# Kernel tuning notes

Hardware: AMD Instinct MI355X
Metric: run time of the kernel (lower is better)

The kernel has to match this reference:

```python
import jax, jax.numpy as jnp
import numpy as np

B, T, C = 2, 2048, 2048
N_HEADS = 16
D_HEAD = C // N_HEADS


def setup_inputs() -> dict:
    key = jax.random.key(0)
    k1, k2, k3 = jax.random.split(key, 3)
    x = jax.random.normal(k1, (B, T, C), dtype=jnp.float32)
    # torch Linear weights stored as [out,in]; we store transposed [in,out] for x @ W
    Wqkv = jax.random.normal(k2, (C, 3 * C), dtype=jnp.float32) * (C ** -0.5)
    Wout = jax.random.normal(k3, (C, C), dtype=jnp.float32) * (C ** -0.5)
    # causal mask: scores where mask==0 are set to -inf
    mask = jnp.tril(jnp.ones((T, T), dtype=bool))[None, None]  # [1,1,T,T]
    return {"x": x, "mask": mask, "Wqkv": Wqkv, "Wout": Wout}


def reference(x, mask, Wqkv, Wout):
    Bx, Tx, Cx = x.shape
    qkv = x @ Wqkv                                   # [B,T,3C]
    q, k, v = jnp.split(qkv, 3, axis=-1)

    def split_heads(t):
        return t.reshape(Bx, Tx, N_HEADS, D_HEAD).transpose(0, 2, 1, 3)  # [B,H,T,Dh]

    q, k, v = split_heads(q), split_heads(k), split_heads(v)
    scale = D_HEAD ** -0.5
    scores = jnp.einsum('bhqd,bhkd->bhqk', q, k) * scale   # [B,H,T,T]
    scores = jnp.where(mask, scores, -jnp.inf)
    attn = jax.nn.softmax(scores, axis=-1)
    # dropout p=0.0 -> identity
    out = jnp.einsum('bhqk,bhkd->bhqd', attn, v)           # [B,H,T,Dh]
    out = out.transpose(0, 2, 1, 3).reshape(Bx, Tx, Cx)
    return out @ Wout
```

## Files before the change

kernel.cpp:

```cpp
#include <hip/hip_runtime.h>
#include <stdint.h>

typedef __bf16 bf16x8 __attribute__((ext_vector_type(8)));
typedef float f32x4 __attribute__((ext_vector_type(4)));
typedef unsigned short u16x8 __attribute__((ext_vector_type(8)));
typedef unsigned int u32x4 __attribute__((ext_vector_type(4)));

__device__ __forceinline__ unsigned short f2bf(float f) {
    unsigned int u = __builtin_bit_cast(unsigned int, f);
    unsigned int r = u + 0x7fffu + ((u >> 16) & 1u);
    return (unsigned short)(r >> 16);
}

__device__ __forceinline__ unsigned int cvt_pk_bf16(float a, float b) {
    unsigned int r;
    asm("v_cvt_pk_bf16_f32 %0, %1, %2" : "=v"(r) : "v"(a), "v"(b));
    return r;
}

__device__ __forceinline__ void async16(const void* g, void* l) {
    __builtin_amdgcn_global_load_lds(
        (const __attribute__((address_space(1))) void*)g,
        (__attribute__((address_space(3))) void*)l, 16, 0, 0);
}


__device__ __forceinline__ void cast_body(
    const float* __restrict__ src, unsigned short* __restrict__ dst, int i)
{
    const float* f = src + (size_t)i * 8;
    f32x4 a = *reinterpret_cast<const f32x4*>(f);
    f32x4 b = *reinterpret_cast<const f32x4*>(f + 4);
    u16x8 r;
    r[0]=f2bf(a[0]); r[1]=f2bf(a[1]); r[2]=f2bf(a[2]); r[3]=f2bf(a[3]);
    r[4]=f2bf(b[0]); r[5]=f2bf(b[1]); r[6]=f2bf(b[2]); r[7]=f2bf(b[3]);
    *reinterpret_cast<u16x8*>(dst + (size_t)i * 8) = r;
}

__device__ __forceinline__ void tcast_body(
    const float* __restrict__ src, unsigned short* __restrict__ dst,
    int R, int Cc, int bx, int by, int tid, unsigned short* St)
{
    const int r0 = by * 64, c0 = bx * 64;
    const int lr  = tid >> 2;
    const int lcb = (tid & 3) * 16;
    const float* sp = src + (size_t)(r0 + lr) * Cc + c0 + lcb;
    #pragma unroll
    for (int u = 0; u < 4; u++) {
        f32x4 v = *reinterpret_cast<const f32x4*>(sp + 4 * u);
        #pragma unroll
        for (int e = 0; e < 4; e++) {
            int c = lcb + 4 * u + e;
            St[c * 64 + (((lr >> 3) ^ ((c >> 4) & 3)) << 3) + (lr & 7)] = f2bf(v[e]);
        }
    }
    __syncthreads();
    #pragma unroll
    for (int i = 0; i < 2; i++) {
        int ck = tid + 256 * i;
        int c = ck >> 3, ch = ck & 7;
        u16x8 val = *reinterpret_cast<const u16x8*>(&St[c * 64 + ((ch ^ ((c >> 4) & 3)) << 3)]);
        *reinterpret_cast<u16x8*>(dst + (size_t)(c0 + c) * R + r0 + ch * 8) = val;
    }
}

__device__ __forceinline__ void vtrans_body(
    const unsigned short* __restrict__ qkv, unsigned short* __restrict__ VT,
    int tx, int dy, int bh, int tid, unsigned short* St)
{
    const int T = 2048, CH = 6144;
    const int b = bh >> 4, h = bh & 15;
    const int t0 = tx * 64, d0 = dy * 64;
    const int lr  = tid >> 2;
    const int lcb = (tid & 3) * 16;
    const unsigned short* sp = qkv + (size_t)(b * T + t0 + lr) * CH + 4096 + h * 128 + d0 + lcb;
    u16x8 v0 = *reinterpret_cast<const u16x8*>(sp);
    u16x8 v1 = *reinterpret_cast<const u16x8*>(sp + 8);
    #pragma unroll
    for (int e = 0; e < 8; e++) {
        int c = lcb + e;
        St[c * 64 + (((lr >> 3) ^ ((c >> 4) & 3)) << 3) + (lr & 7)] = v0[e];
        c = lcb + 8 + e;
        St[c * 64 + (((lr >> 3) ^ ((c >> 4) & 3)) << 3) + (lr & 7)] = v1[e];
    }
    __syncthreads();
    #pragma unroll
    for (int i = 0; i < 2; i++) {
        int ck = tid + 256 * i;
        int d = ck >> 3, ch = ck & 7;
        const int Q = ch & 3, B32 = ch >> 2;
        u16x8 val;
        #pragma unroll
        for (int e = 0; e < 4; e++) {
            int ta = 32 * B32 + 4 * Q + e;
            int tb = ta + 16;
            val[e]     = St[d * 64 + (((ta >> 3) ^ ((d >> 4) & 3)) << 3) + (ta & 7)];
            val[4 + e] = St[d * 64 + (((tb >> 3) ^ ((d >> 4) & 3)) << 3) + (tb & 7)];
        }
        *reinterpret_cast<u16x8*>(VT + (size_t)(bh * 128 + d0 + d) * T + t0 + ch * 8) = val;
    }
}

__global__ __launch_bounds__(256) void prep1(
    const float* __restrict__ x, unsigned short* __restrict__ xb,
    const float* __restrict__ Wqkv, unsigned short* __restrict__ WqkvT)
{
    __shared__ unsigned short St[64 * 64];
    const int bid = blockIdx.x, tid = threadIdx.x;
    if (bid < 4096) {
        cast_body(x, xb, bid * 256 + tid);
    } else {
        const int b2 = bid - 4096;
        tcast_body(Wqkv, WqkvT, 2048, 6144, b2 % 96, b2 / 96, tid, St);
    }
}

__global__ __launch_bounds__(256) void prep2(
    const unsigned short* __restrict__ qkv, unsigned short* __restrict__ VT,
    const float* __restrict__ Wout, unsigned short* __restrict__ WoutT)
{
    __shared__ unsigned short St[64 * 64];
    const int bid = blockIdx.x, tid = threadIdx.x;
    if (bid < 2048) {
        vtrans_body(qkv, VT, bid % 32, (bid >> 5) & 1, bid >> 6, tid, St);
    } else {
        const int b2 = bid - 2048;
        tcast_body(Wout, WoutT, 2048, 2048, b2 % 32, b2 / 32, tid, St);
    }
}

__global__ __launch_bounds__(256) void gemm_bt(
    const unsigned short* __restrict__ A,
    const unsigned short* __restrict__ BT,
    void* __restrict__ C, int M, int N, int K, int cF32)
{
    __shared__ unsigned short As[2][128 * 32];
    __shared__ unsigned short Bs[2][128 * 32];
    const int tid = threadIdx.x;
    const int w = tid >> 6, lane = tid & 63;
    const int quad = lane >> 4, l16 = lane & 15;
    const int wm = (w >> 1) * 64, wn = (w & 1) * 64;
    const int m0 = blockIdx.y * 128, n0 = blockIdx.x * 128;

    const int srow = w * 16 + (lane >> 2);
    const int scol = ((lane & 3) ^ ((lane >> 3) & 3)) * 8;
    const unsigned short* aG = A  + (size_t)(m0 + srow) * K + scol;
    const unsigned short* bG = BT + (size_t)(n0 + srow) * K + scol;
    const int ldsO = (w * 16) * 32;

    const int kch = (quad ^ ((l16 >> 1) & 3)) * 8;

    f32x4 acc[4][4] = {};
    const int nkt = K >> 5;

    async16(aG, &As[0][ldsO]);
    async16(aG + (size_t)64 * K, &As[0][ldsO + 64 * 32]);
    async16(bG, &Bs[0][ldsO]);
    async16(bG + (size_t)64 * K, &Bs[0][ldsO + 64 * 32]);
    asm volatile("s_waitcnt vmcnt(0)\n\ts_barrier" ::: "memory");

    int ct = 0;
    for (int t = 0; t < nkt; ++t) {
        if (t + 1 < nkt) {
            const int k1 = (t + 1) * 32;
            async16(aG + k1, &As[ct ^ 1][ldsO]);
            async16(aG + (size_t)64 * K + k1, &As[ct ^ 1][ldsO + 64 * 32]);
            async16(bG + k1, &Bs[ct ^ 1][ldsO]);
            async16(bG + (size_t)64 * K + k1, &Bs[ct ^ 1][ldsO + 64 * 32]);
        }

        bf16x8 af[4], bf[4];
        #pragma unroll
        for (int i = 0; i < 4; i++)
            af[i] = *reinterpret_cast<const bf16x8*>(&As[ct][(wm + i * 16 + l16) * 32 + kch]);
        #pragma unroll
        for (int c = 0; c < 4; c++)
            bf[c] = *reinterpret_cast<const bf16x8*>(&Bs[ct][(wn + c * 16 + l16) * 32 + kch]);

        __builtin_amdgcn_s_setprio(1);
        #pragma unroll
        for (int i = 0; i < 4; i++)
            #pragma unroll
            for (int c = 0; c < 4; c++)
                acc[i][c] = __builtin_amdgcn_mfma_f32_16x16x32_bf16(af[i], bf[c], acc[i][c], 0, 0, 0);
        __builtin_amdgcn_s_setprio(0);

        asm volatile("s_waitcnt vmcnt(0) lgkmcnt(0)\n\ts_barrier" ::: "memory");
        ct ^= 1;
    }

    #pragma unroll
    for (int i = 0; i < 4; i++)
        #pragma unroll
        for (int c = 0; c < 4; c++)
            #pragma unroll
            for (int r = 0; r < 4; r++) {
                const int row = m0 + wm + i * 16 + quad * 4 + r;
                const int col = n0 + wn + c * 16 + l16;
                const size_t off = (size_t)row * N + col;
                if (cF32) ((float*)C)[off] = acc[i][c][r];
                else ((unsigned short*)C)[off] = f2bf(acc[i][c][r]);
            }
}

__global__ __launch_bounds__(256, 2) void flash_attn(
    const unsigned short* __restrict__ qkv,
    const unsigned short* __restrict__ VT,
    unsigned short* __restrict__ Out)
{
    const int T = 2048, CH = 6144;
    __shared__ unsigned short KsBuf[2][64 * 128];
    __shared__ unsigned short VtBuf[2][128 * 64];

    const int tid = threadIdx.x;
    const int w = tid >> 6, lane = tid & 63;
    const int quad = lane >> 4, l16 = lane & 15;
    const int bh = blockIdx.y, b = bh >> 4, h = bh & 15;
    const int q0 = (gridDim.x - 1 - blockIdx.x) * 128;

    const float sc = 0.08838834764831845f * 1.4426950408889634f;
    const float NINF = -__builtin_inff();

    bf16x8 qf[2][4];
    #pragma unroll
    for (int st = 0; st < 2; st++) {
        const unsigned short* qrow = qkv + (size_t)(b * T + q0 + w * 32 + st * 16 + l16) * CH + h * 128;
        #pragma unroll
        for (int dc = 0; dc < 4; dc++) {
            u16x8 raw = *reinterpret_cast<const u16x8*>(qrow + dc * 32 + quad * 8);
            u16x8 scl;
            #pragma unroll
            for (int e = 0; e < 8; e++) {
                float f = __builtin_bit_cast(float, (unsigned int)raw[e] << 16);
                scl[e] = f2bf(f * sc);
            }
            qf[st][dc] = __builtin_bit_cast(bf16x8, scl);
        }
    }

    f32x4 o[2][8] = {};
    float m_i[2] = {NINF, NINF};
    float l_i[2] = {0.f, 0.f};
    const int xsw = l16 & 7;

    const int kRow = (lane >> 4);
    const int kCh  = lane & 15;
    const int vRow = (lane >> 3);
    const int vCh  = lane & 7;

    auto stageKV = [&](int kv0, unsigned short* kp, unsigned short* vp) {
        #pragma unroll
        for (int i = 0; i < 4; i++) {
            const int r0 = i * 16 + w * 4;
            const int kv = r0 + kRow;
            const int ch = kCh ^ (kv & 7);
            async16(qkv + (size_t)(b * T + kv0 + kv) * CH + 2048 + h * 128 + ch * 8,
                    kp + r0 * 128);
        }
        #pragma unroll
        for (int i = 0; i < 4; i++) {
            const int r0 = i * 32 + w * 8;
            const int d = r0 + vRow;
            const int ch = vCh ^ (d & 7);
            async16(VT + ((size_t)bh * 128 + d) * T + kv0 + ch * 8,
                    vp + r0 * 64);
        }
    };

    unsigned short* kc = KsBuf[0];
    unsigned short* vc = VtBuf[0];
    unsigned short* kn = KsBuf[1];
    unsigned short* vn = VtBuf[1];

    const int nt = (q0 + 128) / 64;

    stageKV(0, kc, vc);
    asm volatile("s_waitcnt vmcnt(0)\n\ts_barrier" ::: "memory");

    for (int t = 0; t < nt; ++t) {
        const int kv0 = t * 64;
        if (t + 1 < nt) stageKV((t + 1) * 64, kn, vn);

        f32x4 s[2][4] = {};
        __builtin_amdgcn_s_setprio(1);
        #pragma unroll
        for (int dc = 0; dc < 4; dc++)
            #pragma unroll
            for (int ntt = 0; ntt < 4; ntt++) {
                bf16x8 kf = *reinterpret_cast<const bf16x8*>(
                    &kc[(ntt * 16 + l16) * 128 + (((dc * 4 + quad) ^ xsw) << 3)]);
                s[0][ntt] = __builtin_amdgcn_mfma_f32_16x16x32_bf16(kf, qf[0][dc], s[0][ntt], 0, 0, 0);
                s[1][ntt] = __builtin_amdgcn_mfma_f32_16x16x32_bf16(kf, qf[1][dc], s[1][ntt], 0, 0, 0);
            }
        __builtin_amdgcn_s_setprio(0);

        unsigned int pk[2][4][2];
        #pragma unroll
        for (int st = 0; st < 2; st++) {
            const int qs = q0 + w * 32 + st * 16;
            const int qrow = qs + l16;
            if (kv0 + 63 > qs) {
                #pragma unroll
                for (int ntt = 0; ntt < 4; ntt++)
                    #pragma unroll
                    for (int r = 0; r < 4; r++)
                        if (kv0 + ntt * 16 + quad * 4 + r > qrow) s[st][ntt][r] = NINF;
            }
            float mx = fmaxf(fmaxf(fmaxf(s[st][0][0], s[st][0][1]), fmaxf(s[st][0][2], s[st][0][3])),
                             fmaxf(fmaxf(s[st][1][0], s[st][1][1]), fmaxf(s[st][1][2], s[st][1][3])));
            mx = fmaxf(mx,
                 fmaxf(fmaxf(fmaxf(s[st][2][0], s[st][2][1]), fmaxf(s[st][2][2], s[st][2][3])),
                       fmaxf(fmaxf(s[st][3][0], s[st][3][1]), fmaxf(s[st][3][2], s[st][3][3]))));
            mx = fmaxf(mx, __shfl_xor(mx, 16));
            mx = fmaxf(mx, __shfl_xor(mx, 32));

            const float mold = m_i[st];
            if (!__all(mx <= mold + 8.0f)) {
                const float mnew = fmaxf(mold, mx);
                const float alpha = exp2f(mold - mnew);
                m_i[st] = mnew;
                l_i[st] *= alpha;
                #pragma unroll
                for (int r = 0; r < 4; r++) {
                    const float a = __shfl(alpha, quad * 4 + r);
                    #pragma unroll
                    for (int c = 0; c < 8; c++) o[st][c][r] *= a;
                }
            }
            const float m = m_i[st];
            float p[4][4];
            #pragma unroll
            for (int ntt = 0; ntt < 4; ntt++)
                #pragma unroll
                for (int r = 0; r < 4; r++)
                    p[ntt][r] = exp2f(s[st][ntt][r] - m);
            float ps = ((p[0][0] + p[0][1]) + (p[0][2] + p[0][3]))
                     + ((p[1][0] + p[1][1]) + (p[1][2] + p[1][3]))
                     + ((p[2][0] + p[2][1]) + (p[2][2] + p[2][3]))
                     + ((p[3][0] + p[3][1]) + (p[3][2] + p[3][3]));
            ps += __shfl_xor(ps, 16);
            ps += __shfl_xor(ps, 32);
            l_i[st] += ps;
            #pragma unroll
            for (int ntt = 0; ntt < 4; ntt++) {
                pk[st][ntt][0] = cvt_pk_bf16(p[ntt][0], p[ntt][1]);
                pk[st][ntt][1] = cvt_pk_bf16(p[ntt][2], p[ntt][3]);
            }
        }

        __builtin_amdgcn_s_setprio(1);
        #pragma unroll
        for (int kc2 = 0; kc2 < 2; kc2++) {
            u32x4 a0, a1;
            a0[0] = pk[0][2*kc2][0];   a0[1] = pk[0][2*kc2][1];
            a0[2] = pk[0][2*kc2+1][0]; a0[3] = pk[0][2*kc2+1][1];
            a1[0] = pk[1][2*kc2][0];   a1[1] = pk[1][2*kc2][1];
            a1[2] = pk[1][2*kc2+1][0]; a1[3] = pk[1][2*kc2+1][1];
            const bf16x8 pf0 = __builtin_bit_cast(bf16x8, a0);
            const bf16x8 pf1 = __builtin_bit_cast(bf16x8, a1);
            #pragma unroll
            for (int c = 0; c < 8; c++) {
                bf16x8 vf = *reinterpret_cast<const bf16x8*>(
                    &vc[(c * 16 + l16) * 64 + (((kc2 * 4 + quad) ^ xsw) << 3)]);
                o[0][c] = __builtin_amdgcn_mfma_f32_16x16x32_bf16(pf0, vf, o[0][c], 0, 0, 0);
                o[1][c] = __builtin_amdgcn_mfma_f32_16x16x32_bf16(pf1, vf, o[1][c], 0, 0, 0);
            }
        }
        __builtin_amdgcn_s_setprio(0);

        asm volatile("s_waitcnt vmcnt(0) lgkmcnt(0)\n\ts_barrier" ::: "memory");

        unsigned short* tp;
        tp = kc; kc = kn; kn = tp;
        tp = vc; vc = vn; vn = tp;
    }

    #pragma unroll
    for (int st = 0; st < 2; st++)
        #pragma unroll
        for (int r = 0; r < 4; r++) {
            const float linv = 1.0f / __shfl(l_i[st], quad * 4 + r);
            const int row = q0 + w * 32 + st * 16 + quad * 4 + r;
            const size_t base = (size_t)(b * T + row) * 2048 + h * 128;
            #pragma unroll
            for (int c = 0; c < 8; c++)
                Out[base + c * 16 + l16] = f2bf(o[st][c][r] * linv);
        }
}

extern "C" void kernel_launch(void* const* d_in, const int* in_sizes, int n_in,
                              void* d_out, int out_size, void* d_ws, size_t ws_size,
                              hipStream_t stream) {
    const int B = 2, T = 2048, C = 2048;
    const float* x    = (const float*)d_in[0];
    const float* Wqkv = (const float*)d_in[2];
    const float* Wout = (const float*)d_in[3];
    const int M = B * T;

    char* ws = (char*)d_ws;
    unsigned short* qkv   = (unsigned short*)ws;
    unsigned short* xb    = (unsigned short*)(ws + 50331648);
    unsigned short* WoutT = xb;
    unsigned short* WqkvT = (unsigned short*)(ws + 67108864);
    unsigned short* VTp   = WqkvT;
    unsigned short* O     = (unsigned short*)(ws + 92274688);

    prep1<<<dim3(4096 + 3072), 256, 0, stream>>>(x, xb, Wqkv, WqkvT);
    gemm_bt<<<dim3(3 * C / 128, M / 128), 256, 0, stream>>>(xb, WqkvT, qkv, M, 3 * C, C, 0);
    prep2<<<dim3(2048 + 1024), 256, 0, stream>>>(qkv, VTp, Wout, WoutT);
    flash_attn<<<dim3(T / 128, B * 16), 256, 0, stream>>>(qkv, VTp, O);
    gemm_bt<<<dim3(C / 128, M / 128), 256, 0, stream>>>(O, WoutT, d_out, M, C, C, 1);
}
```

Measured before the change: 416.6 us.

## Add 256x256-tile triple-buffered GEMM for the QKV projection

Adds a new 512-thread GEMM kernel that computes 256x256 output tiles using 96KB of dynamic LDS with a three-stage async global-to-LDS pipeline. A and B staging is split across the two halves of each k-step so MFMA work overlaps the loads. It is used for the QKV projection when the larger LDS allocation can be set, with the old 128x128 kernel as fallback. The intent is more operand reuse per tile and better latency hiding. The cost is fewer blocks (192 for the 4096x6144 output), which may leave parts of the GPU idle or unevenly loaded.

```diff
diff --git a/kernel.cpp b/kernel.cpp
--- a/kernel.cpp
+++ b/kernel.cpp
@@ -200,6 +200,115 @@
                 const size_t off = (size_t)row * N + col;
                 if (cF32) ((float*)C)[off] = acc[i][c][r];
                 else ((unsigned short*)C)[off] = f2bf(acc[i][c][r]);
+            }
+}
+
+__global__ __launch_bounds__(512) void gemm256r(
+    const unsigned short* __restrict__ A,
+    const unsigned short* __restrict__ BT,
+    unsigned short* __restrict__ Cb,
+    int M, int N, int K)
+{
+    extern __shared__ unsigned short lds[];
+    const int tid = threadIdx.x;
+    const int w = tid >> 6, lane = tid & 63;
+    const int quad = lane >> 4, l16 = lane & 15;
+    const int wm = w >> 2, wn = w & 3;
+    const int m0 = blockIdx.y * 256, n0 = blockIdx.x * 256;
+    const int nkt = K >> 5;
+
+    const int sRow = w * 16 + (lane >> 2);
+    const int sCol = ((lane & 3) ^ ((lane >> 3) & 3)) * 8;
+    const unsigned short* aG = A  + (size_t)(m0 + sRow) * K + sCol;
+    const unsigned short* bG = BT + (size_t)(n0 + sRow) * K + sCol;
+    const int ldsW = w * 512;
+
+    const int kch = (quad ^ ((l16 >> 1) & 3)) * 8;
+    const int aRow0 = wm * 128 + l16;
+    const int bRow0 = wn * 64 + l16;
+
+    f32x4 acc[8][4] = {};
+
+    unsigned short* const Ab0 = lds;
+    unsigned short* const Bb0 = lds + 24576;
+
+    {
+        #pragma unroll
+        for (int t0 = 0; t0 < 2; t0++) {
+            const int k0 = t0 * 32;
+            async16(aG + k0, Ab0 + t0 * 8192 + ldsW);
+            async16(aG + (size_t)128 * K + k0, Ab0 + t0 * 8192 + 4096 + ldsW);
+            async16(bG + k0, Bb0 + t0 * 8192 + ldsW);
+            async16(bG + (size_t)128 * K + k0, Bb0 + t0 * 8192 + 4096 + ldsW);
+        }
+    }
+    asm volatile("s_waitcnt vmcnt(4)\n\ts_barrier" ::: "memory");
+
+    int rb = 0, rs = 2;
+    for (int t = 0; t < nkt; ++t) {
+        const unsigned short* Ac = Ab0 + rb * 8192;
+        const unsigned short* Bc = Bb0 + rb * 8192;
+        const bool doStage = (t + 2 < nkt);
+        const int k2 = (t + 2) * 32;
+
+        if (doStage) {
+            async16(aG + k2, Ab0 + rs * 8192 + ldsW);
+            async16(aG + (size_t)128 * K + k2, Ab0 + rs * 8192 + 4096 + ldsW);
+        }
+        bf16x8 af[4], bf[4];
+        #pragma unroll
+        for (int i = 0; i < 4; i++)
+            af[i] = *reinterpret_cast<const bf16x8*>(Ac + (aRow0 + i * 16) * 32 + kch);
+        #pragma unroll
+        for (int c = 0; c < 4; c++)
+            bf[c] = *reinterpret_cast<const bf16x8*>(Bc + (bRow0 + c * 16) * 32 + kch);
+        asm volatile("s_barrier" ::: "memory");
+        asm volatile("s_waitcnt lgkmcnt(0)" ::: "memory");
+        __builtin_amdgcn_s_setprio(1);
+        #pragma unroll
+        for (int i = 0; i < 4; i++)
+            #pragma unroll
+            for (int c = 0; c < 4; c++)
+                acc[i][c] = __builtin_amdgcn_mfma_f32_16x16x32_bf16(af[i], bf[c], acc[i][c], 0, 0, 0);
+        __builtin_amdgcn_s_setprio(0);
+        asm volatile("s_barrier" ::: "memory");
+
+        if (doStage) {
+            async16(bG + k2, Bb0 + rs * 8192 + ldsW);
+            async16(bG + (size_t)128 * K + k2, Bb0 + rs * 8192 + 4096 + ldsW);
+        }
+        bf16x8 ag[4];
+        #pragma unroll
+        for (int i = 0; i < 4; i++)
+            ag[i] = *reinterpret_cast<const bf16x8*>(Ac + (aRow0 + (i + 4) * 16) * 32 + kch);
+        asm volatile("s_barrier" ::: "memory");
+        asm volatile("s_waitcnt lgkmcnt(0)" ::: "memory");
+        __builtin_amdgcn_s_setprio(1);
+        #pragma unroll
+        for (int i = 0; i < 4; i++)
+            #pragma unroll
+            for (int c = 0; c < 4; c++)
+                acc[i + 4][c] = __builtin_amdgcn_mfma_f32_16x16x32_bf16(ag[i], bf[c], acc[i + 4][c], 0, 0, 0);
+        __builtin_amdgcn_s_setprio(0);
+
+        if (doStage)
+            asm volatile("s_waitcnt vmcnt(4)\n\ts_barrier" ::: "memory");
+        else
+            asm volatile("s_waitcnt vmcnt(0)\n\ts_barrier" ::: "memory");
+
+        rb = (rb == 2) ? 0 : rb + 1;
+        rs = (rs == 2) ? 0 : rs + 1;
+    }
+
+    #pragma unroll
+    for (int i = 0; i < 8; i++)
+        #pragma unroll
+        for (int c = 0; c < 4; c++)
+            #pragma unroll
+            for (int r = 0; r < 4; r++) {
+                const int row = m0 + wm * 128 + i * 16 + quad * 4 + r;
+                const int col = n0 + wn * 64 + c * 16 + l16;
+                Cb[(size_t)row * N + col] = f2bf(acc[i][c][r]);
             }
 }
 
@@ -405,8 +514,19 @@
     unsigned short* VTp   = WqkvT;
     unsigned short* O     = (unsigned short*)(ws + 92274688);
 
+    static int bigLds = 0;
+    if (bigLds == 0) {
+        hipError_t rc = hipFuncSetAttribute(
+            reinterpret_cast<const void*>(gemm256r),
+            hipFuncAttributeMaxDynamicSharedMemorySize, 98304);
+        bigLds = (rc == hipSuccess) ? 1 : -1;
+    }
+
     prep1<<<dim3(4096 + 3072), 256, 0, stream>>>(x, xb, Wqkv, WqkvT);
-    gemm_bt<<<dim3(3 * C / 128, M / 128), 256, 0, stream>>>(xb, WqkvT, qkv, M, 3 * C, C, 0);
+    if (bigLds == 1)
+        gemm256r<<<dim3(3 * C / 256, M / 256), 512, 98304, stream>>>(xb, WqkvT, qkv, M, 3 * C, C);
+    else
+        gemm_bt<<<dim3(3 * C / 128, M / 128), 256, 0, stream>>>(xb, WqkvT, qkv, M, 3 * C, C, 0);
     prep2<<<dim3(2048 + 1024), 256, 0, stream>>>(qkv, VTp, Wout, WoutT);
     flash_attn<<<dim3(T / 128, B * 16), 256, 0, stream>>>(qkv, VTp, O);
     gemm_bt<<<dim3(C / 128, M / 128), 256, 0, stream>>>(O, WoutT, d_out, M, C, C, 1);
```

After: 420.6 us. Within noise of the previous version (+1.0%).

## Fuse V transpose into QKV GEMM epilogue and skip fully masked wave tiles

Applied to the files above, without the earlier changes.

The QKV GEMM epilogue now writes the V columns straight into the transposed per-head VT layout in the permuted t-order that flash attention expects. Q and K are stored in a narrower 4096-column buffer, so the separate V-transpose pass in prep2 and its extra read and write of V go away. Flash attention also skips the QK^T, softmax and PV work for waves whose whole 32-row query slice lies before the current KV tile, while still taking part in the barrier. The cost is 8-byte strided epilogue stores for V in place of coalesced row writes, and some wave imbalance inside each block.

```diff
diff --git a/kernel.cpp b/kernel.cpp
--- a/kernel.cpp
+++ b/kernel.cpp
@@ -4,6 +4,7 @@
 typedef __bf16 bf16x8 __attribute__((ext_vector_type(8)));
 typedef float f32x4 __attribute__((ext_vector_type(4)));
 typedef unsigned short u16x8 __attribute__((ext_vector_type(8)));
+typedef unsigned short u16x4 __attribute__((ext_vector_type(4)));
 typedef unsigned int u32x4 __attribute__((ext_vector_type(4)));
 
 __device__ __forceinline__ unsigned short f2bf(float f) {
@@ -64,43 +65,6 @@
     }
 }
 
-__device__ __forceinline__ void vtrans_body(
-    const unsigned short* __restrict__ qkv, unsigned short* __restrict__ VT,
-    int tx, int dy, int bh, int tid, unsigned short* St)
-{
-    const int T = 2048, CH = 6144;
-    const int b = bh >> 4, h = bh & 15;
-    const int t0 = tx * 64, d0 = dy * 64;
-    const int lr  = tid >> 2;
-    const int lcb = (tid & 3) * 16;
-    const unsigned short* sp = qkv + (size_t)(b * T + t0 + lr) * CH + 4096 + h * 128 + d0 + lcb;
-    u16x8 v0 = *reinterpret_cast<const u16x8*>(sp);
-    u16x8 v1 = *reinterpret_cast<const u16x8*>(sp + 8);
-    #pragma unroll
-    for (int e = 0; e < 8; e++) {
-        int c = lcb + e;
-        St[c * 64 + (((lr >> 3) ^ ((c >> 4) & 3)) << 3) + (lr & 7)] = v0[e];
-        c = lcb + 8 + e;
-        St[c * 64 + (((lr >> 3) ^ ((c >> 4) & 3)) << 3) + (lr & 7)] = v1[e];
-    }
-    __syncthreads();
-    #pragma unroll
-    for (int i = 0; i < 2; i++) {
-        int ck = tid + 256 * i;
-        int d = ck >> 3, ch = ck & 7;
-        const int Q = ch & 3, B32 = ch >> 2;
-        u16x8 val;
-        #pragma unroll
-        for (int e = 0; e < 4; e++) {
-            int ta = 32 * B32 + 4 * Q + e;
-            int tb = ta + 16;
-            val[e]     = St[d * 64 + (((ta >> 3) ^ ((d >> 4) & 3)) << 3) + (ta & 7)];
-            val[4 + e] = St[d * 64 + (((tb >> 3) ^ ((d >> 4) & 3)) << 3) + (tb & 7)];
-        }
-        *reinterpret_cast<u16x8*>(VT + (size_t)(bh * 128 + d0 + d) * T + t0 + ch * 8) = val;
-    }
-}
-
 __global__ __launch_bounds__(256) void prep1(
     const float* __restrict__ x, unsigned short* __restrict__ xb,
     const float* __restrict__ Wqkv, unsigned short* __restrict__ WqkvT)
@@ -116,23 +80,18 @@
 }
 
 __global__ __launch_bounds__(256) void prep2(
-    const unsigned short* __restrict__ qkv, unsigned short* __restrict__ VT,
     const float* __restrict__ Wout, unsigned short* __restrict__ WoutT)
 {
     __shared__ unsigned short St[64 * 64];
     const int bid = blockIdx.x, tid = threadIdx.x;
-    if (bid < 2048) {
-        vtrans_body(qkv, VT, bid % 32, (bid >> 5) & 1, bid >> 6, tid, St);
-    } else {
-        const int b2 = bid - 2048;
-        tcast_body(Wout, WoutT, 2048, 2048, b2 % 32, b2 / 32, tid, St);
-    }
+    tcast_body(Wout, WoutT, 2048, 2048, bid % 32, bid / 32, tid, St);
 }
 
 __global__ __launch_bounds__(256) void gemm_bt(
     const unsigned short* __restrict__ A,
     const unsigned short* __restrict__ BT,
-    void* __restrict__ C, int M, int N, int K, int cF32)
+    void* __restrict__ C, int M, int N, int K, int cF32, int ldc,
+    unsigned short* __restrict__ VTd)
 {
     __shared__ unsigned short As[2][128 * 32];
     __shared__ unsigned short Bs[2][128 * 32];
@@ -189,18 +148,40 @@
         ct ^= 1;
     }
 
-    #pragma unroll
-    for (int i = 0; i < 4; i++)
-        #pragma unroll
-        for (int c = 0; c < 4; c++)
-            #pragma unroll
-            for (int r = 0; r < 4; r++) {
-                const int row = m0 + wm + i * 16 + quad * 4 + r;
-                const int col = n0 + wn + c * 16 + l16;
-                const size_t off = (size_t)row * N + col;
-                if (cF32) ((float*)C)[off] = acc[i][c][r];
-                else ((unsigned short*)C)[off] = f2bf(acc[i][c][r]);
+    if (VTd != nullptr && n0 >= 4096) {
+        const int h = (n0 - 4096) >> 7;
+        #pragma unroll
+        for (int i = 0; i < 4; i++) {
+            const int row = m0 + wm + i * 16 + quad * 4;
+            const int b = row >> 11;
+            const int t64 = (row & 2047) & ~63;
+            const int p = (i >> 1) * 32 + quad * 8 + (i & 1) * 4;
+            #pragma unroll
+            for (int c = 0; c < 4; c++) {
+                const int d = wn + c * 16 + l16;
+                u16x4 val;
+                val[0] = f2bf(acc[i][c][0]);
+                val[1] = f2bf(acc[i][c][1]);
+                val[2] = f2bf(acc[i][c][2]);
+                val[3] = f2bf(acc[i][c][3]);
+                *reinterpret_cast<u16x4*>(
+                    VTd + ((size_t)((b * 16 + h) * 128 + d)) * 2048 + t64 + p) = val;
             }
+        }
+    } else {
+        #pragma unroll
+        for (int i = 0; i < 4; i++)
+            #pragma unroll
+            for (int c = 0; c < 4; c++)
+                #pragma unroll
+                for (int r = 0; r < 4; r++) {
+                    const int row = m0 + wm + i * 16 + quad * 4 + r;
+                    const int col = n0 + wn + c * 16 + l16;
+                    const size_t off = (size_t)row * ldc + col;
+                    if (cF32) ((float*)C)[off] = acc[i][c][r];
+                    else ((unsigned short*)C)[off] = f2bf(acc[i][c][r]);
+                }
+    }
 }
 
 __global__ __launch_bounds__(256, 2) void flash_attn(
@@ -208,7 +189,7 @@
     const unsigned short* __restrict__ VT,
     unsigned short* __restrict__ Out)
 {
-    const int T = 2048, CH = 6144;
+    const int T = 2048, CH = 4096;
     __shared__ unsigned short KsBuf[2][64 * 128];
     __shared__ unsigned short VtBuf[2][128 * 64];
 
@@ -281,92 +262,94 @@
         const int kv0 = t * 64;
         if (t + 1 < nt) stageKV((t + 1) * 64, kn, vn);
 
-        f32x4 s[2][4] = {};
-        __builtin_amdgcn_s_setprio(1);
-        #pragma unroll
-        for (int dc = 0; dc < 4; dc++)
-            #pragma unroll
-            for (int ntt = 0; ntt < 4; ntt++) {
-                bf16x8 kf = *reinterpret_cast<const bf16x8*>(
-                    &kc[(ntt * 16 + l16) * 128 + (((dc * 4 + quad) ^ xsw) << 3)]);
-                s[0][ntt] = __builtin_amdgcn_mfma_f32_16x16x32_bf16(kf, qf[0][dc], s[0][ntt], 0, 0, 0);
-                s[1][ntt] = __builtin_amdgcn_mfma_f32_16x16x32_bf16(kf, qf[1][dc], s[1][ntt], 0, 0, 0);
-            }
-        __builtin_amdgcn_s_setprio(0);
-
-        unsigned int pk[2][4][2];
-        #pragma unroll
-        for (int st = 0; st < 2; st++) {
-            const int qs = q0 + w * 32 + st * 16;
-            const int qrow = qs + l16;
-            if (kv0 + 63 > qs) {
+        if (kv0 <= q0 + w * 32 + 31) {
+            f32x4 s[2][4] = {};
+            __builtin_amdgcn_s_setprio(1);
+            #pragma unroll
+            for (int dc = 0; dc < 4; dc++)
+                #pragma unroll
+                for (int ntt = 0; ntt < 4; ntt++) {
+                    bf16x8 kf = *reinterpret_cast<const bf16x8*>(
+                        &kc[(ntt * 16 + l16) * 128 + (((dc * 4 + quad) ^ xsw) << 3)]);
+                    s[0][ntt] = __builtin_amdgcn_mfma_f32_16x16x32_bf16(kf, qf[0][dc], s[0][ntt], 0, 0, 0);
+                    s[1][ntt] = __builtin_amdgcn_mfma_f32_16x16x32_bf16(kf, qf[1][dc], s[1][ntt], 0, 0, 0);
+                }
+            __builtin_amdgcn_s_setprio(0);
+
+            unsigned int pk[2][4][2];
+            #pragma unroll
+            for (int st = 0; st < 2; st++) {
+                const int qs = q0 + w * 32 + st * 16;
+                const int qrow = qs + l16;
+                if (kv0 + 63 > qs) {
+                    #pragma unroll
+                    for (int ntt = 0; ntt < 4; ntt++)
+                        #pragma unroll
+                        for (int r = 0; r < 4; r++)
+                            if (kv0 + ntt * 16 + quad * 4 + r > qrow) s[st][ntt][r] = NINF;
+                }
+                float mx = fmaxf(fmaxf(fmaxf(s[st][0][0], s[st][0][1]), fmaxf(s[st][0][2], s[st][0][3])),
+                                 fmaxf(fmaxf(s[st][1][0], s[st][1][1]), fmaxf(s[st][1][2], s[st][1][3])));
+                mx = fmaxf(mx,
+                     fmaxf(fmaxf(fmaxf(s[st][2][0], s[st][2][1]), fmaxf(s[st][2][2], s[st][2][3])),
+                           fmaxf(fmaxf(s[st][3][0], s[st][3][1]), fmaxf(s[st][3][2], s[st][3][3]))));
+                mx = fmaxf(mx, __shfl_xor(mx, 16));
+                mx = fmaxf(mx, __shfl_xor(mx, 32));
+
+                const float mold = m_i[st];
+                if (!__all(mx <= mold + 8.0f)) {
+                    const float mnew = fmaxf(mold, mx);
+                    const float alpha = exp2f(mold - mnew);
+                    m_i[st] = mnew;
+                    l_i[st] *= alpha;
+                    #pragma unroll
+                    for (int r = 0; r < 4; r++) {
+                        const float a = __shfl(alpha, quad * 4 + r);
+                        #pragma unroll
+                        for (int c = 0; c < 8; c++) o[st][c][r] *= a;
+                    }
+                }
+                const float m = m_i[st];
+                float p[4][4];
                 #pragma unroll
                 for (int ntt = 0; ntt < 4; ntt++)
                     #pragma unroll
                     for (int r = 0; r < 4; r++)
-                        if (kv0 + ntt * 16 + quad * 4 + r > qrow) s[st][ntt][r] = NINF;
+                        p[ntt][r] = exp2f(s[st][ntt][r] - m);
+                float ps = ((p[0][0] + p[0][1]) + (p[0][2] + p[0][3]))
+                         + ((p[1][0] + p[1][1]) + (p[1][2] + p[1][3]))
+                         + ((p[2][0] + p[2][1]) + (p[2][2] + p[2][3]))
+                         + ((p[3][0] + p[3][1]) + (p[3][2] + p[3][3]));
+                ps += __shfl_xor(ps, 16);
+                ps += __shfl_xor(ps, 32);
+                l_i[st] += ps;
+                #pragma unroll
+                for (int ntt = 0; ntt < 4; ntt++) {
+                    pk[st][ntt][0] = cvt_pk_bf16(p[ntt][0], p[ntt][1]);
+                    pk[st][ntt][1] = cvt_pk_bf16(p[ntt][2], p[ntt][3]);
+                }
             }
-            float mx = fmaxf(fmaxf(fmaxf(s[st][0][0], s[st][0][1]), fmaxf(s[st][0][2], s[st][0][3])),
-                             fmaxf(fmaxf(s[st][1][0], s[st][1][1]), fmaxf(s[st][1][2], s[st][1][3])));
-            mx = fmaxf(mx,
-                 fmaxf(fmaxf(fmaxf(s[st][2][0], s[st][2][1]), fmaxf(s[st][2][2], s[st][2][3])),
-                       fmaxf(fmaxf(s[st][3][0], s[st][3][1]), fmaxf(s[st][3][2], s[st][3][3]))));
-            mx = fmaxf(mx, __shfl_xor(mx, 16));
-            mx = fmaxf(mx, __shfl_xor(mx, 32));
-
-            const float mold = m_i[st];
-            if (!__all(mx <= mold + 8.0f)) {
-                const float mnew = fmaxf(mold, mx);
-                const float alpha = exp2f(mold - mnew);
-                m_i[st] = mnew;
-                l_i[st] *= alpha;
-                #pragma unroll
-                for (int r = 0; r < 4; r++) {
-                    const float a = __shfl(alpha, quad * 4 + r);
-                    #pragma unroll
-                    for (int c = 0; c < 8; c++) o[st][c][r] *= a;
+
+            __builtin_amdgcn_s_setprio(1);
+            #pragma unroll
+            for (int kc2 = 0; kc2 < 2; kc2++) {
+                u32x4 a0, a1;
+                a0[0] = pk[0][2*kc2][0];   a0[1] = pk[0][2*kc2][1];
+                a0[2] = pk[0][2*kc2+1][0]; a0[3] = pk[0][2*kc2+1][1];
+                a1[0] = pk[1][2*kc2][0];   a1[1] = pk[1][2*kc2][1];
+                a1[2] = pk[1][2*kc2+1][0]; a1[3] = pk[1][2*kc2+1][1];
+                const bf16x8 pf0 = __builtin_bit_cast(bf16x8, a0);
+                const bf16x8 pf1 = __builtin_bit_cast(bf16x8, a1);
+                #pragma unroll
+                for (int c = 0; c < 8; c++) {
+                    bf16x8 vf = *reinterpret_cast<const bf16x8*>(
+                        &vc[(c * 16 + l16) * 64 + (((kc2 * 4 + quad) ^ xsw) << 3)]);
+                    o[0][c] = __builtin_amdgcn_mfma_f32_16x16x32_bf16(pf0, vf, o[0][c], 0, 0, 0);
+                    o[1][c] = __builtin_amdgcn_mfma_f32_16x16x32_bf16(pf1, vf, o[1][c], 0, 0, 0);
                 }
             }
-            const float m = m_i[st];
-            float p[4][4];
-            #pragma unroll
-            for (int ntt = 0; ntt < 4; ntt++)
-                #pragma unroll
-                for (int r = 0; r < 4; r++)
-                    p[ntt][r] = exp2f(s[st][ntt][r] - m);
-            float ps = ((p[0][0] + p[0][1]) + (p[0][2] + p[0][3]))
-                     + ((p[1][0] + p[1][1]) + (p[1][2] + p[1][3]))
-                     + ((p[2][0] + p[2][1]) + (p[2][2] + p[2][3]))
-                     + ((p[3][0] + p[3][1]) + (p[3][2] + p[3][3]));
-            ps += __shfl_xor(ps, 16);
-            ps += __shfl_xor(ps, 32);
-            l_i[st] += ps;
-            #pragma unroll
-            for (int ntt = 0; ntt < 4; ntt++) {
-                pk[st][ntt][0] = cvt_pk_bf16(p[ntt][0], p[ntt][1]);
-                pk[st][ntt][1] = cvt_pk_bf16(p[ntt][2], p[ntt][3]);
-            }
-        }
-
-        __builtin_amdgcn_s_setprio(1);
-        #pragma unroll
-        for (int kc2 = 0; kc2 < 2; kc2++) {
-            u32x4 a0, a1;
-            a0[0] = pk[0][2*kc2][0];   a0[1] = pk[0][2*kc2][1];
-            a0[2] = pk[0][2*kc2+1][0]; a0[3] = pk[0][2*kc2+1][1];
-            a1[0] = pk[1][2*kc2][0];   a1[1] = pk[1][2*kc2][1];
-            a1[2] = pk[1][2*kc2+1][0]; a1[3] = pk[1][2*kc2+1][1];
-            const bf16x8 pf0 = __builtin_bit_cast(bf16x8, a0);
-            const bf16x8 pf1 = __builtin_bit_cast(bf16x8, a1);
-            #pragma unroll
-            for (int c = 0; c < 8; c++) {
-                bf16x8 vf = *reinterpret_cast<const bf16x8*>(
-                    &vc[(c * 16 + l16) * 64 + (((kc2 * 4 + quad) ^ xsw) << 3)]);
-                o[0][c] = __builtin_amdgcn_mfma_f32_16x16x32_bf16(pf0, vf, o[0][c], 0, 0, 0);
-                o[1][c] = __builtin_amdgcn_mfma_f32_16x16x32_bf16(pf1, vf, o[1][c], 0, 0, 0);
-            }
-        }
-        __builtin_amdgcn_s_setprio(0);
+            __builtin_amdgcn_s_setprio(0);
+        }
 
         asm volatile("s_waitcnt vmcnt(0) lgkmcnt(0)\n\ts_barrier" ::: "memory");
 
@@ -398,16 +381,18 @@
     const int M = B * T;
 
     char* ws = (char*)d_ws;
-    unsigned short* qkv   = (unsigned short*)ws;
-    unsigned short* xb    = (unsigned short*)(ws + 50331648);
+    unsigned short* qkvQK = (unsigned short*)ws;
+    unsigned short* xb    = (unsigned short*)(ws + 33554432);
     unsigned short* WoutT = xb;
-    unsigned short* WqkvT = (unsigned short*)(ws + 67108864);
-    unsigned short* VTp   = WqkvT;
+    unsigned short* WqkvT = (unsigned short*)(ws + 50331648);
+    unsigned short* VTp   = (unsigned short*)(ws + 75497472);
     unsigned short* O     = (unsigned short*)(ws + 92274688);
 
     prep1<<<dim3(4096 + 3072), 256, 0, stream>>>(x, xb, Wqkv, WqkvT);
-    gemm_bt<<<dim3(3 * C / 128, M / 128), 256, 0, stream>>>(xb, WqkvT, qkv, M, 3 * C, C, 0);
-    prep2<<<dim3(2048 + 1024), 256, 0, stream>>>(qkv, VTp, Wout, WoutT);
-    flash_attn<<<dim3(T / 128, B * 16), 256, 0, stream>>>(qkv, VTp, O);
-    gemm_bt<<<dim3(C / 128, M / 128), 256, 0, stream>>>(O, WoutT, d_out, M, C, C, 1);
-}
+    gemm_bt<<<dim3(3 * C / 128, M / 128), 256, 0, stream>>>(
+        xb, WqkvT, qkvQK, M, 3 * C, C, 0, 4096, VTp);
+    prep2<<<dim3(1024), 256, 0, stream>>>(Wout, WoutT);
+    flash_attn<<<dim3(T / 128, B * 16), 256, 0, stream>>>(qkvQK, VTp, O);
+    gemm_bt<<<dim3(C / 128, M / 128), 256, 0, stream>>>(
+        O, WoutT, d_out, M, C, C, 1, C, nullptr);
+}
```

After: 406.8 us. 1.02x faster.
